# Kernel optimization log

Hardware: AMD Instinct MI355X
Metric: run time of the kernel (lower is better)

## Reference

```python
import jax, jax.numpy as jnp
import numpy as np

# Module hyperparameters (from init_kwargs)
B, C, E, T = 8, 128, 128, 128          # batch, in_channels, embedding(freq), time
O, G, KW, KS = 256, 4, 9, 1            # out_channels, groups, kernel_width, kernel_stride
D = C // G                              # kernel depth per group = 32
N = O // G                              # filters per group = 64
AH, AS = 2, 2                           # activate_height, activate_stride
NEG_SLOPE = 0.01                        # nn.LeakyReLU default


def setup_inputs() -> dict:
    key = jax.random.key(0)
    kx, kw = jax.random.split(key)
    x = jax.random.normal(kx, (B, C, E, T), dtype=jnp.float32)
    # xavier_uniform over (O, D, E, KW): fan_in = D*E*KW, fan_out = O*E*KW
    fan_in, fan_out = D * E * KW, O * E * KW
    limit = float(np.sqrt(6.0 / (fan_in + fan_out)))
    weight = jax.random.uniform(kw, (O, D, E, KW), dtype=jnp.float32,
                                minval=-limit, maxval=limit)
    return {"x": x, "weight": weight}


def reference(x, weight):
    b, c, e, t = x.shape
    # --- symmetric-ish zero pad along time so unfold yields exactly t windows ---
    pad = (t - 1) * KS - t + KW
    xp = jnp.pad(x, ((0, 0), (0, 0), (0, 0), (pad // 2, (pad + 1) // 2)))
    # --- unfold: windows of size KW at stride KS -> (b, c, e, t, KW) ---
    idx = jnp.arange(t)[:, None] * KS + jnp.arange(KW)[None, :]  # (t, KW)
    xu = xp[..., idx]                                            # (b, c, e, t, KW)
    # --- grouped linear-conv: instead of materializing (b,t,g,n,d,e,KW), contract d,KW ---
    xu = xu.reshape(b, G, D, e, t, KW)                 # (b, g, d, e, t, w)
    wr = weight.reshape(G, N, D, e, KW)                # (g, n, d, e, w)
    # z[b,g,n,e,t] = sum_{d,w} xu * wr  (the all-ones conv sums over d and full width w)
    z = jnp.einsum('bgdetw,gndew->bgnet', xu, wr).reshape(b, O, e, t)
    # --- all-ones conv height pooling: kernel AH, stride AS over e (valid) ---
    f_out = (e - AH) // AS + 1
    cs = jnp.cumsum(z, axis=2)
    cs = jnp.concatenate([jnp.zeros_like(cs[:, :, :1]), cs], axis=2)  # prefix sums
    pos = jnp.arange(f_out) * AS
    pooled = cs[:, :, pos + AH, :] - cs[:, :, pos, :]   # (b, O, f_out, t)
    # --- LeakyReLU ---
    y = jnp.where(pooled >= 0, pooled, NEG_SLOPE * pooled)
    return y  # (b, o, f_out, t), matching 'b o f t'
```

## Files before the change

### kernel.cpp

```cpp
#include <hip/hip_runtime.h>
#include <cstddef>

typedef __attribute__((ext_vector_type(8))) short short8v;
typedef __attribute__((ext_vector_type(4))) short short4v;
typedef __attribute__((ext_vector_type(4))) float f32x4;

__device__ __forceinline__ unsigned short f2bf(float f) {
    unsigned u = __float_as_uint(f);
    u = (u + 0x7FFFu + ((u >> 16) & 1u)) >> 16;
    return (unsigned short)u;
}

__global__ __launch_bounds__(256) void prep_w(const float* __restrict__ w,
                                              unsigned short* __restrict__ wb)
{
    const int g  = blockIdx.x >> 6;
    const int f  = blockIdx.x & 63;
    const int e0 = 2 * f;
    const int tid = threadIdx.x;
    __shared__ unsigned short ls[64 * 580];

    #pragma unroll 4
    for (int i = 0; i < 72; ++i) {
        int fl  = tid + i * 256;
        int od  = fl / 9;
        int f2i = fl - od * 9;
        int o_l = od >> 5;
        int d   = od & 31;
        const float2 v = *reinterpret_cast<const float2*>(
            &w[(size_t)((g * 64 + o_l) * 32 + d) * 1152 + e0 * 9 + f2i * 2]);
        ushort2 hh; hh.x = f2bf(v.x); hh.y = f2bf(v.y);
        *reinterpret_cast<ushort2*>(&ls[o_l * 580 + d * 18 + f2i * 2]) = hh;
    }
    __syncthreads();

    unsigned short* wo = wb + (size_t)(g * 64 + f) * 36864;
    #pragma unroll 2
    for (int i = 0; i < 18; ++i) {
        int oc   = tid + i * 256;
        int ks   = oc >> 8;
        int nt   = (oc >> 6) & 3;
        int lane = oc & 63;
        int li = lane & 15, hi = lane >> 4;
        int e  = (ks >= 9) ? 1 : 0;
        int w9 = ks - 9 * e;
        int o_l = nt * 16 + li;
        short8v vv;
        #pragma unroll
        for (int j = 0; j < 8; ++j)
            vv[j] = (short)ls[o_l * 580 + (hi * 8 + j) * 18 + e * 9 + w9];
        *reinterpret_cast<short8v*>(&wo[(size_t)oc * 8]) = vv;
    }
}

__global__ __launch_bounds__(256, 1) void lconv_mfma(const float* __restrict__ x,
                                                     const unsigned short* __restrict__ wb,
                                                     float* __restrict__ out)
{
    extern __shared__ __align__(16) unsigned short smem[];
    unsigned short* As = smem;
    unsigned short* xs = smem + 36864;

    const int g  = blockIdx.x >> 6;
    const int f  = blockIdx.x & 63;
    const int e0 = 2 * f;

    const int tid  = threadIdx.x;
    const int lane = tid & 63;
    const int wv   = tid >> 6;
    const int bl   = wv & 1;
    const int th   = wv >> 1;
    const int li   = lane & 15;
    const int hi   = lane >> 4;
    const int t    = tid & 127;
    const int z    = tid >> 7;

    const unsigned short* wslab = wb + (size_t)(g * 64 + f) * 36864;

    #pragma unroll
    for (int i = 0; i < 18; ++i) {
        int off = i * 2048 + wv * 512 + lane * 8;
        __builtin_amdgcn_global_load_lds(
            (const __attribute__((address_space(1))) void*)(wslab + off),
            (__attribute__((address_space(3))) void*)(As + i * 2048 + wv * 512),
            16, 0, 0);
    }

    float xr[32];
    auto issueX = [&](int p, int e) {
        const int b = p * 2 + z;
        const float* xp0 = &x[((size_t)(b * 128 + g * 32) * 128 + (e0 + e)) * 128 + t];
        #pragma unroll
        for (int d = 0; d < 32; ++d)
            xr[d] = xp0[(size_t)d * 16384];
    };
    auto lwriteX = [&](int e) {
        unsigned short* base = xs + (e * 2 + z) * 5440;
        #pragma unroll
        for (int dq = 0; dq < 8; ++dq) {
            short4v hq;
            hq[0] = (short)f2bf(xr[dq * 4 + 0]);
            hq[1] = (short)f2bf(xr[dq * 4 + 1]);
            hq[2] = (short)f2bf(xr[dq * 4 + 2]);
            hq[3] = (short)f2bf(xr[dq * 4 + 3]);
            *reinterpret_cast<short4v*>(&base[(t + 4) * 40 + dq * 4]) = hq;
        }
    };

    {
        int e  = tid >> 7;
        int b2 = (tid >> 6) & 1;
        int r  = (tid >> 3) & 7;
        int dq = tid & 7;
        int tp = (r < 4) ? r : (128 + r);
        short4v zz = {0, 0, 0, 0};
        *reinterpret_cast<short4v*>(&xs[(e * 2 + b2) * 5440 + tp * 40 + dq * 4]) = zz;
    }

    issueX(0, 0); lwriteX(0);
    issueX(0, 1); lwriteX(1);
    issueX(1, 0);
    __syncthreads();

    f32x4 acc[4][4];
    #pragma unroll
    for (int nt = 0; nt < 4; ++nt)
        #pragma unroll
        for (int tt = 0; tt < 4; ++tt)
            acc[nt][tt] = (f32x4){0.f, 0.f, 0.f, 0.f};

    auto compute = [&](int e) {
        const unsigned short* xb = xs + (e * 2 + bl) * 5440;
        #pragma unroll
        for (int w9 = 0; w9 < 9; ++w9) {
            short8v Af[4], Bf[4];
            #pragma unroll
            for (int nt = 0; nt < 4; ++nt)
                Af[nt] = *reinterpret_cast<const short8v*>(
                    &As[(e * 9 + w9) * 2048 + nt * 512 + lane * 8]);
            #pragma unroll
            for (int tt = 0; tt < 4; ++tt) {
                int tp = th * 64 + tt * 16 + li + w9;
                Bf[tt] = *reinterpret_cast<const short8v*>(&xb[tp * 40 + hi * 8]);
            }
            __builtin_amdgcn_s_setprio(1);
            #pragma unroll
            for (int nt = 0; nt < 4; ++nt)
                #pragma unroll
                for (int tt = 0; tt < 4; ++tt)
                    acc[nt][tt] = __builtin_amdgcn_mfma_f32_16x16x32_bf16(
                        Af[nt], Bf[tt], acc[nt][tt], 0, 0, 0);
            __builtin_amdgcn_s_setprio(0);
        }
    };

    for (int p = 0; p < 4; ++p) {
        compute(0);
        __syncthreads();
        if (p < 3) {
            lwriteX(0);
            issueX(p + 1, 1);
            __builtin_amdgcn_sched_barrier(0);
        }
        compute(1);
        __syncthreads();
        if (p < 3) lwriteX(1);
        if (p < 2) {
            issueX(p + 2, 0);
            __builtin_amdgcn_sched_barrier(0);
        }

        const int b = p * 2 + bl;
        #pragma unroll
        for (int nt = 0; nt < 4; ++nt)
            #pragma unroll
            for (int tt = 0; tt < 4; ++tt)
                #pragma unroll
                for (int j = 0; j < 4; ++j) {
                    float v = acc[nt][tt][j];
                    v = (v >= 0.f) ? v : 0.01f * v;
                    int n  = nt * 16 + hi * 4 + j;
                    int tc = th * 64 + tt * 16 + li;
                    out[(((size_t)(b * 256 + g * 64 + n)) * 64 + f) * 128 + tc] = v;
                    acc[nt][tt][j] = 0.f;
                }
    }
}

extern "C" void kernel_launch(void* const* d_in, const int* in_sizes, int n_in,
                              void* d_out, int out_size, void* d_ws, size_t ws_size,
                              hipStream_t stream)
{
    const float* x = (const float*)d_in[0];
    const float* w = (const float*)d_in[1];
    float* out = (float*)d_out;
    unsigned short* wb = (unsigned short*)d_ws;

    (void)hipFuncSetAttribute((const void*)lconv_mfma,
                              hipFuncAttributeMaxDynamicSharedMemorySize, 117248);

    hipLaunchKernelGGL(prep_w, dim3(256), dim3(256), 0, stream, w, wb);
    hipLaunchKernelGGL(lconv_mfma, dim3(256), dim3(256), 117248, stream, x, wb, out);
}
```

Baseline: 53.88 us.

## Give each wave a private x tile and two batches, dropping block barriers

The x staging buffer is split so each wave owns its own LDS region and processes two whole batches across the full 128-wide time axis. Each wave now holds 4x8 accumulator tiles instead of 4x4. Block-wide __syncthreads in the main loop are replaced by per-wave software pipelining, and x is loaded as float2 for wider global reads. In exchange the kernel uses more LDS (about 157 KB) and more registers for accumulators and prefetch buffers, which could cause spills or worse scheduling.

Result: no change. 53.31 us (-1.1%).

```diff
diff --git a/kernel.cpp b/kernel.cpp
--- a/kernel.cpp
+++ b/kernel.cpp
@@ -59,7 +59,6 @@
 {
     extern __shared__ __align__(16) unsigned short smem[];
     unsigned short* As = smem;
-    unsigned short* xs = smem + 36864;
 
     const int g  = blockIdx.x >> 6;
     const int f  = blockIdx.x & 63;
@@ -68,123 +67,119 @@
     const int tid  = threadIdx.x;
     const int lane = tid & 63;
     const int wv   = tid >> 6;
-    const int bl   = wv & 1;
-    const int th   = wv >> 1;
     const int li   = lane & 15;
     const int hi   = lane >> 4;
-    const int t    = tid & 127;
-    const int z    = tid >> 7;
+
+    unsigned short* xsw = smem + 36864 + wv * 10880;
 
     const unsigned short* wslab = wb + (size_t)(g * 64 + f) * 36864;
-
     #pragma unroll
     for (int i = 0; i < 18; ++i) {
-        int off = i * 2048 + wv * 512 + lane * 8;
         __builtin_amdgcn_global_load_lds(
-            (const __attribute__((address_space(1))) void*)(wslab + off),
-            (__attribute__((address_space(3))) void*)(As + i * 2048 + wv * 512),
+            (const __attribute__((address_space(1))) void*)(wslab + i * 2048 + tid * 8),
+            (__attribute__((address_space(3))) void*)(As + i * 2048 + tid * 8),
             16, 0, 0);
     }
 
-    float xr[32];
-    auto issueX = [&](int p, int e) {
-        const int b = p * 2 + z;
-        const float* xp0 = &x[((size_t)(b * 128 + g * 32) * 128 + (e0 + e)) * 128 + t];
+    #pragma unroll
+    for (int it = 0; it < 3; ++it) {
+        int u = it * 64 + lane;
+        if (u < 160) {
+            int e  = u / 80;
+            int r  = (u % 80) / 10;
+            int dq = u % 10;
+            int tp = (r < 4) ? r : (128 + r);
+            short4v zz = {0, 0, 0, 0};
+            *reinterpret_cast<short4v*>(&xsw[e * 5440 + tp * 40 + dq * 4]) = zz;
+        }
+    }
+
+    float2 fr[32];
+    auto issueX = [&](int b, int e) {
+        const float* xp0 = &x[((size_t)(b * 128 + g * 32) * 128 + (e0 + e)) * 128 + 2 * lane];
         #pragma unroll
         for (int d = 0; d < 32; ++d)
-            xr[d] = xp0[(size_t)d * 16384];
+            fr[d] = *reinterpret_cast<const float2*>(xp0 + (size_t)d * 16384);
     };
     auto lwriteX = [&](int e) {
-        unsigned short* base = xs + (e * 2 + z) * 5440;
+        unsigned short* base = xsw + e * 5440 + (2 * lane + 4) * 40;
         #pragma unroll
         for (int dq = 0; dq < 8; ++dq) {
-            short4v hq;
-            hq[0] = (short)f2bf(xr[dq * 4 + 0]);
-            hq[1] = (short)f2bf(xr[dq * 4 + 1]);
-            hq[2] = (short)f2bf(xr[dq * 4 + 2]);
-            hq[3] = (short)f2bf(xr[dq * 4 + 3]);
-            *reinterpret_cast<short4v*>(&base[(t + 4) * 40 + dq * 4]) = hq;
+            short4v h0, h1;
+            #pragma unroll
+            for (int j = 0; j < 4; ++j) {
+                h0[j] = (short)f2bf(fr[dq * 4 + j].x);
+                h1[j] = (short)f2bf(fr[dq * 4 + j].y);
+            }
+            *reinterpret_cast<short4v*>(&base[dq * 4])      = h0;
+            *reinterpret_cast<short4v*>(&base[40 + dq * 4]) = h1;
         }
     };
 
-    {
-        int e  = tid >> 7;
-        int b2 = (tid >> 6) & 1;
-        int r  = (tid >> 3) & 7;
-        int dq = tid & 7;
-        int tp = (r < 4) ? r : (128 + r);
-        short4v zz = {0, 0, 0, 0};
-        *reinterpret_cast<short4v*>(&xs[(e * 2 + b2) * 5440 + tp * 40 + dq * 4]) = zz;
-    }
-
-    issueX(0, 0); lwriteX(0);
-    issueX(0, 1); lwriteX(1);
-    issueX(1, 0);
+    const int b0 = wv, b1 = wv + 4;
+    issueX(b0, 0); lwriteX(0);
+    issueX(b0, 1); lwriteX(1);
     __syncthreads();
 
-    f32x4 acc[4][4];
+    f32x4 acc[4][8];
     #pragma unroll
     for (int nt = 0; nt < 4; ++nt)
         #pragma unroll
-        for (int tt = 0; tt < 4; ++tt)
+        for (int tt = 0; tt < 8; ++tt)
             acc[nt][tt] = (f32x4){0.f, 0.f, 0.f, 0.f};
 
-    auto compute = [&](int e) {
-        const unsigned short* xb = xs + (e * 2 + bl) * 5440;
+    auto compute_half = [&](int e) {
         #pragma unroll
         for (int w9 = 0; w9 < 9; ++w9) {
-            short8v Af[4], Bf[4];
+            short8v Af[4], Bf[8];
             #pragma unroll
             for (int nt = 0; nt < 4; ++nt)
                 Af[nt] = *reinterpret_cast<const short8v*>(
                     &As[(e * 9 + w9) * 2048 + nt * 512 + lane * 8]);
             #pragma unroll
-            for (int tt = 0; tt < 4; ++tt) {
-                int tp = th * 64 + tt * 16 + li + w9;
-                Bf[tt] = *reinterpret_cast<const short8v*>(&xb[tp * 40 + hi * 8]);
+            for (int tt = 0; tt < 8; ++tt) {
+                int tp = tt * 16 + li + w9;
+                Bf[tt] = *reinterpret_cast<const short8v*>(
+                    &xsw[e * 5440 + tp * 40 + hi * 8]);
             }
             __builtin_amdgcn_s_setprio(1);
             #pragma unroll
             for (int nt = 0; nt < 4; ++nt)
                 #pragma unroll
-                for (int tt = 0; tt < 4; ++tt)
+                for (int tt = 0; tt < 8; ++tt)
                     acc[nt][tt] = __builtin_amdgcn_mfma_f32_16x16x32_bf16(
                         Af[nt], Bf[tt], acc[nt][tt], 0, 0, 0);
             __builtin_amdgcn_s_setprio(0);
         }
     };
 
-    for (int p = 0; p < 4; ++p) {
-        compute(0);
-        __syncthreads();
-        if (p < 3) {
-            lwriteX(0);
-            issueX(p + 1, 1);
-            __builtin_amdgcn_sched_barrier(0);
-        }
-        compute(1);
-        __syncthreads();
-        if (p < 3) lwriteX(1);
-        if (p < 2) {
-            issueX(p + 2, 0);
-            __builtin_amdgcn_sched_barrier(0);
-        }
-
-        const int b = p * 2 + bl;
+    auto store_b = [&](int b) {
         #pragma unroll
         for (int nt = 0; nt < 4; ++nt)
             #pragma unroll
-            for (int tt = 0; tt < 4; ++tt)
+            for (int tt = 0; tt < 8; ++tt)
                 #pragma unroll
                 for (int j = 0; j < 4; ++j) {
                     float v = acc[nt][tt][j];
                     v = (v >= 0.f) ? v : 0.01f * v;
                     int n  = nt * 16 + hi * 4 + j;
-                    int tc = th * 64 + tt * 16 + li;
+                    int tc = tt * 16 + li;
                     out[(((size_t)(b * 256 + g * 64 + n)) * 64 + f) * 128 + tc] = v;
                     acc[nt][tt][j] = 0.f;
                 }
-    }
+    };
+
+    issueX(b1, 0);
+    compute_half(0);
+    lwriteX(0);
+    issueX(b1, 1);
+    compute_half(1);
+    store_b(b0);
+    lwriteX(1);
+
+    compute_half(0);
+    compute_half(1);
+    store_b(b1);
 }
 
 extern "C" void kernel_launch(void* const* d_in, const int* in_sizes, int n_in,
@@ -197,8 +192,8 @@
     unsigned short* wb = (unsigned short*)d_ws;
 
     (void)hipFuncSetAttribute((const void*)lconv_mfma,
-                              hipFuncAttributeMaxDynamicSharedMemorySize, 117248);
+                              hipFuncAttributeMaxDynamicSharedMemorySize, 160768);
 
     hipLaunchKernelGGL(prep_w, dim3(256), dim3(256), 0, stream, w, wb);
-    hipLaunchKernelGGL(lconv_mfma, dim3(256), dim3(256), 117248, stream, x, wb, out);
+    hipLaunchKernelGGL(lconv_mfma, dim3(256), dim3(256), 160768, stream, x, wb, out);
 }
```
